# Kernel tuning notes

Hardware: AMD Instinct MI355X
Metric: run time of the kernel (lower is better)

## Reference

```python
import jax, jax.numpy as jnp
import numpy as np

N = 100000
E = 1600000
IN_FEATS = 512
H1, F1 = 8, 8          # layer1: 8 heads x 8 units
H2, F2 = 1, 40         # layer2: 1 head x out_feats
NEG_SLOPE = 0.2


def setup_inputs() -> dict:
    key = jax.random.key(0)
    ks = jax.random.split(key, 12)
    x = jax.random.normal(ks[0], (N, IN_FEATS), dtype=jnp.float32)
    src = jax.random.randint(ks[1], (E,), 0, N, dtype=jnp.int32)
    dst = jax.random.randint(ks[2], (E,), 0, N, dtype=jnp.int32)
    # Xavier-ish init for params
    W1 = jax.random.normal(ks[3], (IN_FEATS, H1 * F1), dtype=jnp.float32) * (1.0 / np.sqrt(IN_FEATS))
    al1 = jax.random.normal(ks[4], (H1, F1), dtype=jnp.float32) * 0.1
    ar1 = jax.random.normal(ks[5], (H1, F1), dtype=jnp.float32) * 0.1
    b1 = jnp.zeros((H1 * F1,), dtype=jnp.float32)
    W2 = jax.random.normal(ks[6], (H1 * F1, H2 * F2), dtype=jnp.float32) * (1.0 / np.sqrt(H1 * F1))
    al2 = jax.random.normal(ks[7], (H2, F2), dtype=jnp.float32) * 0.1
    ar2 = jax.random.normal(ks[8], (H2, F2), dtype=jnp.float32) * 0.1
    b2 = jnp.zeros((H2 * F2,), dtype=jnp.float32)
    return {"x": x, "src": src, "dst": dst,
            "W1": W1, "al1": al1, "ar1": ar1, "b1": b1,
            "W2": W2, "al2": al2, "ar2": ar2, "b2": b2}


def _gat_conv(feat, src, dst, W, al, ar, b, activation):
    """DGL-style GATConv (dropout disabled / eval mode)."""
    n = feat.shape[0]
    heads, fdim = al.shape
    h = (feat @ W).reshape(n, heads, fdim)            # [N, H, F]
    el = jnp.einsum('nhf,hf->nh', h, al)              # [N, H]
    er = jnp.einsum('nhf,hf->nh', h, ar)              # [N, H]
    e = jax.nn.leaky_relu(el[src] + er[dst], NEG_SLOPE)   # [E, H]
    # edge softmax over incoming edges of each dst node (numerically stable)
    m = jax.ops.segment_max(e, dst, num_segments=n)   # [N, H]
    ex = jnp.exp(e - m[dst])
    s = jax.ops.segment_sum(ex, dst, num_segments=n)  # [N, H]
    alpha = ex / s[dst]                               # [E, H]
    msg = h[src] * alpha[:, :, None]                  # [E, H, F]
    rst = jax.ops.segment_sum(msg, dst, num_segments=n)  # [N, H, F]
    rst = rst + b.reshape(1, heads, fdim)
    if activation is not None:
        rst = activation(rst)
    return rst


def reference(x, src, dst, W1, al1, ar1, b1, W2, al2, ar2, b2):
    h1 = _gat_conv(x, src, dst, W1, al1, ar1, b1, jax.nn.elu)   # [N, H1, F1]
    h1 = h1.reshape(x.shape[0], H1 * F1)                        # flatten(1)
    h2 = _gat_conv(h1, src, dst, W2, al2, ar2, b2, None)        # [N, 1, F2]
    logits = h2.mean(axis=1)                                    # [N, F2]
    return jax.nn.log_softmax(logits, axis=1)
```

## Files before the change

### kernel.cpp

```cpp
#include <hip/hip_runtime.h>
#include <cstdint>
#include <cstddef>

#define IN_F 512
#define C1 64
#define NH 8
#define FD 8
#define C2 40
#define NEG 0.2f

typedef __attribute__((ext_vector_type(8))) short bf16x8;
typedef __attribute__((ext_vector_type(4))) float f32x4;

__device__ inline unsigned short f32_to_bf16_rne(float f) {
    unsigned int u = __float_as_uint(f);
    unsigned int r = (u + 0x7FFFu + ((u >> 16) & 1u)) >> 16;
    return (unsigned short)r;
}
__device__ inline float bf16_to_f32(unsigned short s) {
    return __uint_as_float(((unsigned int)s) << 16);
}

__global__ __launch_bounds__(256) void hist_k(const int* __restrict__ dst, int* __restrict__ deg, int E) {
    int e = blockIdx.x * 256 + threadIdx.x;
    if (e < E) atomicAdd(&deg[dst[e]], 1);
}

__global__ __launch_bounds__(1024) void scan_local_k(const int* __restrict__ deg, int* __restrict__ rowp,
                                                     int* __restrict__ bsums, int n) {
    __shared__ int tmp[1024];
    int tx = threadIdx.x;
    int i = blockIdx.x * 1024 + tx;
    int v = (i < n) ? deg[i] : 0;
    tmp[tx] = v;
    __syncthreads();
    for (int d = 1; d < 1024; d <<= 1) {
        int t = (tx >= d) ? tmp[tx - d] : 0;
        __syncthreads();
        tmp[tx] += t;
        __syncthreads();
    }
    if (i < n) rowp[i] = tmp[tx] - v;
    if (tx == 1023) bsums[blockIdx.x] = tmp[tx];
}

__global__ __launch_bounds__(128) void scan_sums_k(int* bsums, int nb) {
    __shared__ int tmp[128];
    int tx = threadIdx.x;
    int v = (tx < nb) ? bsums[tx] : 0;
    tmp[tx] = v;
    __syncthreads();
    for (int d = 1; d < 128; d <<= 1) {
        int t = (tx >= d) ? tmp[tx - d] : 0;
        __syncthreads();
        tmp[tx] += t;
        __syncthreads();
    }
    if (tx < nb) bsums[tx] = tmp[tx] - v;
}

__global__ __launch_bounds__(1024) void scan_add_k(int* rowp, const int* __restrict__ bsums, int n) {
    int i = blockIdx.x * 1024 + threadIdx.x;
    if (i < n) rowp[i] += bsums[blockIdx.x];
}

__global__ __launch_bounds__(256) void scatter_k(const int* __restrict__ src, const int* __restrict__ dst,
                                                 const int* __restrict__ rowp, int* __restrict__ fill,
                                                 int* __restrict__ csr_src, int E) {
    int e = blockIdx.x * 256 + threadIdx.x;
    if (e >= E) return;
    int d = dst[e];
    int p = atomicAdd(&fill[d], 1);
    csr_src[rowp[d] + p] = src[e];
}

__global__ __launch_bounds__(256) void wt_pre_k(const float* __restrict__ W1,
                                                unsigned short* __restrict__ wt_hi,
                                                unsigned short* __restrict__ wt_lo) {
    int id = blockIdx.x * 256 + threadIdx.x;
    if (id >= IN_F * C1) return;
    int col = id & (C1 - 1);
    int k = id >> 6;
    float w = W1[id];
    unsigned short hb = f32_to_bf16_rne(w);
    unsigned short lb = f32_to_bf16_rne(w - bf16_to_f32(hb));
    wt_hi[(size_t)col * IN_F + k] = hb;
    wt_lo[(size_t)col * IN_F + k] = lb;
}

__global__ __launch_bounds__(256) void gemm1_mfma_k(const float* __restrict__ x,
                                                    const unsigned short* __restrict__ wt_hi,
                                                    const unsigned short* __restrict__ wt_lo,
                                                    float* __restrict__ h, int N) {
    __shared__ alignas(16) unsigned short wlds[2][8192];
    const int tid = threadIdx.x;
    const int wave = tid >> 6, lane = tid & 63;
    const int m = lane & 15, q = lane >> 4;
    const int row = blockIdx.x * 64 + wave * 16 + m;
    const int row_c = row < N ? row : N - 1;
    const float* xp = x + (size_t)row_c * IN_F + q * 8;

    f32x4 acc[4];
#pragma unroll
    for (int ct = 0; ct < 4; ct++) acc[ct] = (f32x4){0.f, 0.f, 0.f, 0.f};
    float4 xr[2][4];

#define WLOAD(c, buf)                                                                              \
    {                                                                                              \
        _Pragma("unroll") for (int j_ = 0; j_ < 4; j_++) {                                         \
            int slot_ = j_ * 256 + wave * 64 + lane;                                               \
            const unsigned short* gbase_ = (slot_ < 512) ? wt_hi : wt_lo;                          \
            int s_ = slot_ & 511;                                                                  \
            int col_ = s_ & 63, kq_ = s_ >> 6;                                                     \
            const unsigned short* g_ = gbase_ + (size_t)col_ * IN_F + (c) * 64 + kq_ * 8;          \
            unsigned short* l_ = &wlds[buf][0] + (size_t)(j_ * 256 + wave * 64) * 8;               \
            __builtin_amdgcn_global_load_lds((const __attribute__((address_space(1))) unsigned int*)g_, \
                                             (__attribute__((address_space(3))) unsigned int*)l_,  \
                                             16, 0, 0);                                            \
        }                                                                                          \
    }
#define XLOAD(c, r)                                  \
    {                                                \
        const float* xsrc_ = xp + (c) * 64;          \
        (r)[0] = *(const float4*)(xsrc_);            \
        (r)[1] = *(const float4*)(xsrc_ + 4);        \
        (r)[2] = *(const float4*)(xsrc_ + 32);       \
        (r)[3] = *(const float4*)(xsrc_ + 36);       \
    }

    WLOAD(0, 0);
    XLOAD(0, xr[0]);

    for (int c = 0; c < 8; c++) {
        int p = c & 1;
        __syncthreads();
        if (c < 7) {
            WLOAD(c + 1, p ^ 1);
            XLOAD(c + 1, xr[p ^ 1]);
        }
#pragma unroll
        for (int ki = 0; ki < 2; ki++) {
            float f[8];
            f[0] = xr[p][ki * 2].x; f[1] = xr[p][ki * 2].y; f[2] = xr[p][ki * 2].z; f[3] = xr[p][ki * 2].w;
            f[4] = xr[p][ki * 2 + 1].x; f[5] = xr[p][ki * 2 + 1].y; f[6] = xr[p][ki * 2 + 1].z; f[7] = xr[p][ki * 2 + 1].w;
            unsigned int u[8], lu[8];
#pragma unroll
            for (int j = 0; j < 8; j++) u[j] = __float_as_uint(f[j]);
            union { uint4 u4; bf16x8 v; } H, L;
            H.u4.x = __builtin_amdgcn_perm(u[1], u[0], 0x07060302u);
            H.u4.y = __builtin_amdgcn_perm(u[3], u[2], 0x07060302u);
            H.u4.z = __builtin_amdgcn_perm(u[5], u[4], 0x07060302u);
            H.u4.w = __builtin_amdgcn_perm(u[7], u[6], 0x07060302u);
#pragma unroll
            for (int j = 0; j < 8; j++)
                lu[j] = __float_as_uint(f[j] - __uint_as_float(u[j] & 0xFFFF0000u));
            L.u4.x = __builtin_amdgcn_perm(lu[1], lu[0], 0x07060302u);
            L.u4.y = __builtin_amdgcn_perm(lu[3], lu[2], 0x07060302u);
            L.u4.z = __builtin_amdgcn_perm(lu[5], lu[4], 0x07060302u);
            L.u4.w = __builtin_amdgcn_perm(lu[7], lu[6], 0x07060302u);
            int kq = ki * 4 + q;
#pragma unroll
            for (int ct = 0; ct < 4; ct++) {
                int slot = kq * 64 + ct * 16 + m;
                bf16x8 bh = *(const bf16x8*)&wlds[p][slot * 8];
                bf16x8 bl = *(const bf16x8*)&wlds[p][4096 + slot * 8];
                acc[ct] = __builtin_amdgcn_mfma_f32_16x16x32_bf16(H.v, bh, acc[ct], 0, 0, 0);
                acc[ct] = __builtin_amdgcn_mfma_f32_16x16x32_bf16(L.v, bh, acc[ct], 0, 0, 0);
                acc[ct] = __builtin_amdgcn_mfma_f32_16x16x32_bf16(H.v, bl, acc[ct], 0, 0, 0);
            }
        }
    }
    int rbase = blockIdx.x * 64 + wave * 16 + q * 4;
#pragma unroll
    for (int r = 0; r < 4; r++) {
        int ro = rbase + r;
        if (ro < N) {
#pragma unroll
            for (int ct = 0; ct < 4; ct++)
                h[(size_t)ro * C1 + ct * 16 + m] = acc[ct][r];
        }
    }
#undef WLOAD
#undef XLOAD
}

__global__ __launch_bounds__(256) void attn1_k(const float* __restrict__ h, const float* __restrict__ al,
                                               const float* __restrict__ ar, float* __restrict__ el,
                                               float* __restrict__ er, int N) {
    int idx = blockIdx.x * 256 + threadIdx.x;
    if (idx >= N * NH) return;
    int n = idx >> 3, hd = idx & 7;
    const float4* hp = (const float4*)(h + (size_t)n * C1 + hd * FD);
    const float4* alp = (const float4*)(al + hd * FD);
    const float4* arp = (const float4*)(ar + hd * FD);
    float4 v0 = hp[0], v1 = hp[1];
    float4 a0 = alp[0], a1 = alp[1];
    float4 r0 = arp[0], r1 = arp[1];
    float e_l = v0.x * a0.x + v0.y * a0.y + v0.z * a0.z + v0.w * a0.w +
                v1.x * a1.x + v1.y * a1.y + v1.z * a1.z + v1.w * a1.w;
    float e_r = v0.x * r0.x + v0.y * r0.y + v0.z * r0.z + v0.w * r0.w +
                v1.x * r1.x + v1.y * r1.y + v1.z * r1.z + v1.w * r1.w;
    el[idx] = e_l;
    er[idx] = e_r;
}

__global__ __launch_bounds__(256) void l1_agg_k(const float* __restrict__ h,
                                                const float* __restrict__ el, const float* __restrict__ er,
                                                const int* __restrict__ rowp, const int* __restrict__ deg,
                                                const int* __restrict__ csr_src, const float* __restrict__ b1,
                                                const float* __restrict__ W2, const float* __restrict__ al2,
                                                const float* __restrict__ ar2,
                                                float* __restrict__ h2pre, float* __restrict__ el2o,
                                                float* __restrict__ er2o, int N) {
    __shared__ float ws[C1 * C2];
    __shared__ float hs[32][C1];
    __shared__ float h2s[32][C2];
    __shared__ float a2s[2 * C2];
    int tid = threadIdx.x;
    for (int i = tid; i < C1 * C2; i += 256) ws[i] = W2[i];
    if (tid < C2) a2s[tid] = al2[tid];
    else if (tid < 2 * C2) a2s[tid] = ar2[tid - C2];

    int n0 = blockIdx.x * 32;
    int ln = tid >> 3;
    int hd = tid & 7;
    int n = n0 + ln;
    float4 acc0 = make_float4(0.f, 0.f, 0.f, 0.f);
    float4 acc1 = make_float4(0.f, 0.f, 0.f, 0.f);
    float s = 0.f;
    if (n < N) {
        int start = rowp[n], cnt = deg[n];
        float erd = er[n * NH + hd];
        int i = 0;
        for (; i + 1 < cnt; i += 2) {
            int sn0 = csr_src[start + i];
            int sn1 = csr_src[start + i + 1];
            float e0 = el[sn0 * NH + hd] + erd;
            float e1 = el[sn1 * NH + hd] + erd;
            e0 = e0 > 0.f ? e0 : NEG * e0;
            e1 = e1 > 0.f ? e1 : NEG * e1;
            float w0 = __expf(e0), w1 = __expf(e1);
            s += w0 + w1;
            const float4* hp0 = (const float4*)(h + (size_t)sn0 * C1 + hd * FD);
            const float4* hp1 = (const float4*)(h + (size_t)sn1 * C1 + hd * FD);
            float4 v00 = hp0[0], v01 = hp0[1];
            float4 v10 = hp1[0], v11 = hp1[1];
            acc0.x += w0 * v00.x + w1 * v10.x; acc0.y += w0 * v00.y + w1 * v10.y;
            acc0.z += w0 * v00.z + w1 * v10.z; acc0.w += w0 * v00.w + w1 * v10.w;
            acc1.x += w0 * v01.x + w1 * v11.x; acc1.y += w0 * v01.y + w1 * v11.y;
            acc1.z += w0 * v01.z + w1 * v11.z; acc1.w += w0 * v01.w + w1 * v11.w;
        }
        if (i < cnt) {
            int sn = csr_src[start + i];
            float e = el[sn * NH + hd] + erd;
            e = e > 0.f ? e : NEG * e;
            float w0 = __expf(e);
            s += w0;
            const float4* hp = (const float4*)(h + (size_t)sn * C1 + hd * FD);
            float4 v0 = hp[0], v1 = hp[1];
            acc0.x += w0 * v0.x; acc0.y += w0 * v0.y; acc0.z += w0 * v0.z; acc0.w += w0 * v0.w;
            acc1.x += w0 * v1.x; acc1.y += w0 * v1.y; acc1.z += w0 * v1.z; acc1.w += w0 * v1.w;
        }
    }
    float sinv = (s > 0.f) ? 1.f / s : 0.f;
    const float4* bp = (const float4*)(b1 + hd * FD);
    float4 bb0 = bp[0], bb1 = bp[1];
    float o[8] = {acc0.x * sinv + bb0.x, acc0.y * sinv + bb0.y, acc0.z * sinv + bb0.z, acc0.w * sinv + bb0.w,
                  acc1.x * sinv + bb1.x, acc1.y * sinv + bb1.y, acc1.z * sinv + bb1.z, acc1.w * sinv + bb1.w};
#pragma unroll
    for (int f = 0; f < 8; f++) o[f] = o[f] > 0.f ? o[f] : (__expf(o[f]) - 1.f);
    *(float4*)&hs[ln][hd * FD] = make_float4(o[0], o[1], o[2], o[3]);
    *(float4*)&hs[ln][hd * FD + 4] = make_float4(o[4], o[5], o[6], o[7]);
    __syncthreads();

    for (int oidx = tid; oidx < 32 * C2; oidx += 256) {
        int r = oidx / C2, c = oidx % C2;
        float sum = 0.f;
#pragma unroll
        for (int k = 0; k < C1; k++) sum += hs[r][k] * ws[k * C2 + c];
        h2s[r][c] = sum;
        int nn = n0 + r;
        if (nn < N) h2pre[(size_t)nn * C2 + c] = sum;
    }
    __syncthreads();

    if (tid < 32) {
        int nn = n0 + tid;
        if (nn < N) {
            float e_l = 0.f, e_r = 0.f;
#pragma unroll
            for (int c = 0; c < C2; c++) {
                float v = h2s[tid][c];
                e_l += v * a2s[c];
                e_r += v * a2s[C2 + c];
            }
            el2o[nn] = e_l;
            er2o[nn] = e_r;
        }
    }
}

__global__ __launch_bounds__(256) void l2_fused_k(const float* __restrict__ h2, const float* __restrict__ el,
                                                  const float* __restrict__ er, const int* __restrict__ rowp,
                                                  const int* __restrict__ deg, const int* __restrict__ csr_src,
                                                  const float* __restrict__ b2, float* __restrict__ out, int N) {
    int tid = threadIdx.x;
    int n = blockIdx.x * 32 + (tid >> 3);
    int sub = tid & 7;
    if (n >= N) return;
    int start = rowp[n], cnt = deg[n];
    float erd = er[n];
    float s = 0.f;
    float4 a4 = make_float4(0.f, 0.f, 0.f, 0.f);
    float a1 = 0.f;
    int i = 0;
    for (; i + 1 < cnt; i += 2) {
        int sn0 = csr_src[start + i];
        int sn1 = csr_src[start + i + 1];
        float e0 = el[sn0] + erd, e1 = el[sn1] + erd;
        e0 = e0 > 0.f ? e0 : NEG * e0;
        e1 = e1 > 0.f ? e1 : NEG * e1;
        float w0 = __expf(e0), w1 = __expf(e1);
        s += w0 + w1;
        const float* hp0 = h2 + (size_t)sn0 * C2;
        const float* hp1 = h2 + (size_t)sn1 * C2;
        float4 v0 = *(const float4*)(hp0 + sub * 4);
        float4 v1 = *(const float4*)(hp1 + sub * 4);
        float s0 = hp0[32 + sub], s1 = hp1[32 + sub];
        a4.x += w0 * v0.x + w1 * v1.x; a4.y += w0 * v0.y + w1 * v1.y;
        a4.z += w0 * v0.z + w1 * v1.z; a4.w += w0 * v0.w + w1 * v1.w;
        a1 += w0 * s0 + w1 * s1;
    }
    if (i < cnt) {
        int sn = csr_src[start + i];
        float e = el[sn] + erd;
        e = e > 0.f ? e : NEG * e;
        float w0 = __expf(e);
        s += w0;
        const float* hp = h2 + (size_t)sn * C2;
        float4 v = *(const float4*)(hp + sub * 4);
        a4.x += w0 * v.x; a4.y += w0 * v.y; a4.z += w0 * v.z; a4.w += w0 * v.w;
        a1 += w0 * hp[32 + sub];
    }
    float sinv = (s > 0.f) ? 1.f / s : 0.f;
    float4 bb = *(const float4*)(b2 + sub * 4);
    a4.x = a4.x * sinv + bb.x; a4.y = a4.y * sinv + bb.y;
    a4.z = a4.z * sinv + bb.z; a4.w = a4.w * sinv + bb.w;
    a1 = a1 * sinv + b2[32 + sub];
    float mx = fmaxf(fmaxf(fmaxf(a4.x, a4.y), fmaxf(a4.z, a4.w)), a1);
#pragma unroll
    for (int off = 1; off < 8; off <<= 1) mx = fmaxf(mx, __shfl_xor(mx, off, 8));
    float se = __expf(a4.x - mx) + __expf(a4.y - mx) + __expf(a4.z - mx) + __expf(a4.w - mx) + __expf(a1 - mx);
#pragma unroll
    for (int off = 1; off < 8; off <<= 1) se += __shfl_xor(se, off, 8);
    float ls = __logf(se) + mx;
    float* op = out + (size_t)n * C2;
    *(float4*)(op + sub * 4) = make_float4(a4.x - ls, a4.y - ls, a4.z - ls, a4.w - ls);
    op[32 + sub] = a1 - ls;
}

extern "C" void kernel_launch(void* const* d_in, const int* in_sizes, int n_in,
                              void* d_out, int out_size, void* d_ws, size_t ws_size,
                              hipStream_t stream) {
    (void)n_in; (void)out_size; (void)ws_size;
    const float* x   = (const float*)d_in[0];
    const int*   src = (const int*)d_in[1];
    const int*   dst = (const int*)d_in[2];
    const float* W1  = (const float*)d_in[3];
    const float* al1 = (const float*)d_in[4];
    const float* ar1 = (const float*)d_in[5];
    const float* b1  = (const float*)d_in[6];
    const float* W2  = (const float*)d_in[7];
    const float* al2 = (const float*)d_in[8];
    const float* ar2 = (const float*)d_in[9];
    const float* b2  = (const float*)d_in[10];
    float* out = (float*)d_out;
    const int N = in_sizes[0] / IN_F;
    const int E = in_sizes[1];

    char* w = (char*)d_ws;
    auto alloc = [&](size_t bytes) -> char* {
        char* p = w;
        w += (bytes + 255) & ~(size_t)255;
        return p;
    };
    int* deg     = (int*)alloc((size_t)N * 4);
    int* fill    = (int*)alloc((size_t)N * 4);
    int* rowp    = (int*)alloc((size_t)N * 4);
    int* bsums   = (int*)alloc(512);
    int* csr_src = (int*)alloc((size_t)E * 4);
    unsigned short* wt_hi = (unsigned short*)alloc((size_t)IN_F * C1 * 2);
    unsigned short* wt_lo = (unsigned short*)alloc((size_t)IN_F * C1 * 2);
    float* h1pre = (float*)alloc((size_t)N * C1 * 4);
    float* el1   = (float*)alloc((size_t)N * NH * 4);
    float* er1   = (float*)alloc((size_t)N * NH * 4);
    float* h2pre = (float*)alloc((size_t)N * C2 * 4);
    float* el2   = (float*)alloc((size_t)N * 4);
    float* er2   = (float*)alloc((size_t)N * 4);

    hipMemsetAsync(deg, 0, (size_t)N * 4, stream);
    hipMemsetAsync(fill, 0, (size_t)N * 4, stream);

    int ebl = (E + 255) / 256;
    int nb = (N + 1023) / 1024;
    hist_k<<<ebl, 256, 0, stream>>>(dst, deg, E);
    scan_local_k<<<nb, 1024, 0, stream>>>(deg, rowp, bsums, N);
    scan_sums_k<<<1, 128, 0, stream>>>(bsums, nb);
    scan_add_k<<<nb, 1024, 0, stream>>>(rowp, bsums, N);
    scatter_k<<<ebl, 256, 0, stream>>>(src, dst, rowp, fill, csr_src, E);

    wt_pre_k<<<(IN_F * C1 + 255) / 256, 256, 0, stream>>>(W1, wt_hi, wt_lo);
    gemm1_mfma_k<<<(N + 63) / 64, 256, 0, stream>>>(x, wt_hi, wt_lo, h1pre, N);
    attn1_k<<<(N * NH + 255) / 256, 256, 0, stream>>>(h1pre, al1, ar1, el1, er1, N);
    l1_agg_k<<<(N + 31) / 32, 256, 0, stream>>>(h1pre, el1, er1, rowp, deg, csr_src, b1,
                                                W2, al2, ar2, h2pre, el2, er2, N);
    l2_fused_k<<<(N + 31) / 32, 256, 0, stream>>>(h2pre, el2, er2, rowp, deg, csr_src, b2, out, N);
}
```

Measured before the change: 648.9 us.

## Split layer-1 aggregation into wave-per-node gather and separate GEMM2 kernel

Layer-1 aggregation now runs one 64-lane wave per destination node, with each lane owning one output channel, so each neighbour row is read as one coalesced 256-byte line. The W2 projection and layer-2 attention logits move into a separate kernel that tiles 64 nodes per block. CSR construction records the atomic slot in the histogram pass, which removes the second atomic pass and the fill buffer. The layer-2 gather loop is unrolled by four to keep more loads in flight. In exchange it adds an N×64 intermediate write and read, an extra kernel launch, an E-sized pos buffer, and redundant el/exp work across the 8 lanes of each head.

```diff
diff --git a/kernel.cpp b/kernel.cpp
--- a/kernel.cpp
+++ b/kernel.cpp
@@ -21,9 +21,10 @@
     return __uint_as_float(((unsigned int)s) << 16);
 }
 
-__global__ __launch_bounds__(256) void hist_k(const int* __restrict__ dst, int* __restrict__ deg, int E) {
+__global__ __launch_bounds__(256) void hist_k(const int* __restrict__ dst, int* __restrict__ deg,
+                                              int* __restrict__ pos, int E) {
     int e = blockIdx.x * 256 + threadIdx.x;
-    if (e < E) atomicAdd(&deg[dst[e]], 1);
+    if (e < E) pos[e] = atomicAdd(&deg[dst[e]], 1);
 }
 
 __global__ __launch_bounds__(1024) void scan_local_k(const int* __restrict__ deg, int* __restrict__ rowp,
@@ -65,13 +66,11 @@
 }
 
 __global__ __launch_bounds__(256) void scatter_k(const int* __restrict__ src, const int* __restrict__ dst,
-                                                 const int* __restrict__ rowp, int* __restrict__ fill,
+                                                 const int* __restrict__ rowp, const int* __restrict__ pos,
                                                  int* __restrict__ csr_src, int E) {
     int e = blockIdx.x * 256 + threadIdx.x;
     if (e >= E) return;
-    int d = dst[e];
-    int p = atomicAdd(&fill[d], 1);
-    csr_src[rowp[d] + p] = src[e];
+    csr_src[rowp[dst[e]] + pos[e]] = src[e];
 }
 
 __global__ __launch_bounds__(256) void wt_pre_k(const float* __restrict__ W1,
@@ -204,77 +203,75 @@
     er[idx] = e_r;
 }
 
-__global__ __launch_bounds__(256) void l1_agg_k(const float* __restrict__ h,
-                                                const float* __restrict__ el, const float* __restrict__ er,
-                                                const int* __restrict__ rowp, const int* __restrict__ deg,
-                                                const int* __restrict__ csr_src, const float* __restrict__ b1,
-                                                const float* __restrict__ W2, const float* __restrict__ al2,
-                                                const float* __restrict__ ar2,
-                                                float* __restrict__ h2pre, float* __restrict__ el2o,
-                                                float* __restrict__ er2o, int N) {
+__global__ __launch_bounds__(256) void l1_wave_k(const float* __restrict__ h,
+                                                 const float* __restrict__ el, const float* __restrict__ er,
+                                                 const int* __restrict__ rowp, const int* __restrict__ deg,
+                                                 const int* __restrict__ csr_src, const float* __restrict__ b1,
+                                                 float* __restrict__ h1out, int N) {
+    int n = (blockIdx.x * 256 + threadIdx.x) >> 6;
+    if (n >= N) return;
+    int lane = threadIdx.x & 63;
+    int hg = lane >> 3;
+    int start = rowp[n], cnt = deg[n];
+    float erd = er[n * NH + hg];
+    float acc = 0.f, s = 0.f;
+    int i = 0;
+    for (; i + 4 <= cnt; i += 4) {
+        const int* cp = csr_src + start + i;
+        int sn0 = cp[0], sn1 = cp[1], sn2 = cp[2], sn3 = cp[3];
+        float e0 = el[sn0 * NH + hg];
+        float e1 = el[sn1 * NH + hg];
+        float e2 = el[sn2 * NH + hg];
+        float e3 = el[sn3 * NH + hg];
+        float v0 = h[(size_t)sn0 * C1 + lane];
+        float v1 = h[(size_t)sn1 * C1 + lane];
+        float v2 = h[(size_t)sn2 * C1 + lane];
+        float v3 = h[(size_t)sn3 * C1 + lane];
+        e0 += erd; e1 += erd; e2 += erd; e3 += erd;
+        e0 = e0 > 0.f ? e0 : NEG * e0;
+        e1 = e1 > 0.f ? e1 : NEG * e1;
+        e2 = e2 > 0.f ? e2 : NEG * e2;
+        e3 = e3 > 0.f ? e3 : NEG * e3;
+        float w0 = __expf(e0), w1 = __expf(e1), w2 = __expf(e2), w3 = __expf(e3);
+        s += (w0 + w1) + (w2 + w3);
+        acc += w0 * v0 + w1 * v1 + w2 * v2 + w3 * v3;
+    }
+    for (; i < cnt; i++) {
+        int sn = csr_src[start + i];
+        float e = el[sn * NH + hg] + erd;
+        e = e > 0.f ? e : NEG * e;
+        float w0 = __expf(e);
+        s += w0;
+        acc += w0 * h[(size_t)sn * C1 + lane];
+    }
+    float sinv = (s > 0.f) ? 1.f / s : 0.f;
+    float o = acc * sinv + b1[lane];
+    o = o > 0.f ? o : (__expf(o) - 1.f);
+    h1out[(size_t)n * C1 + lane] = o;
+}
+
+__global__ __launch_bounds__(256) void gemm2_attn2_k(const float* __restrict__ h1, const float* __restrict__ W2,
+                                                     const float* __restrict__ al2, const float* __restrict__ ar2,
+                                                     float* __restrict__ h2pre, float* __restrict__ el2,
+                                                     float* __restrict__ er2, int N) {
     __shared__ float ws[C1 * C2];
-    __shared__ float hs[32][C1];
-    __shared__ float h2s[32][C2];
+    __shared__ float hs[64][C1];
+    __shared__ float h2s[64][C2];
     __shared__ float a2s[2 * C2];
-    int tid = threadIdx.x;
-    for (int i = tid; i < C1 * C2; i += 256) ws[i] = W2[i];
-    if (tid < C2) a2s[tid] = al2[tid];
-    else if (tid < 2 * C2) a2s[tid] = ar2[tid - C2];
-
-    int n0 = blockIdx.x * 32;
-    int ln = tid >> 3;
-    int hd = tid & 7;
-    int n = n0 + ln;
-    float4 acc0 = make_float4(0.f, 0.f, 0.f, 0.f);
-    float4 acc1 = make_float4(0.f, 0.f, 0.f, 0.f);
-    float s = 0.f;
-    if (n < N) {
-        int start = rowp[n], cnt = deg[n];
-        float erd = er[n * NH + hd];
-        int i = 0;
-        for (; i + 1 < cnt; i += 2) {
-            int sn0 = csr_src[start + i];
-            int sn1 = csr_src[start + i + 1];
-            float e0 = el[sn0 * NH + hd] + erd;
-            float e1 = el[sn1 * NH + hd] + erd;
-            e0 = e0 > 0.f ? e0 : NEG * e0;
-            e1 = e1 > 0.f ? e1 : NEG * e1;
-            float w0 = __expf(e0), w1 = __expf(e1);
-            s += w0 + w1;
-            const float4* hp0 = (const float4*)(h + (size_t)sn0 * C1 + hd * FD);
-            const float4* hp1 = (const float4*)(h + (size_t)sn1 * C1 + hd * FD);
-            float4 v00 = hp0[0], v01 = hp0[1];
-            float4 v10 = hp1[0], v11 = hp1[1];
-            acc0.x += w0 * v00.x + w1 * v10.x; acc0.y += w0 * v00.y + w1 * v10.y;
-            acc0.z += w0 * v00.z + w1 * v10.z; acc0.w += w0 * v00.w + w1 * v10.w;
-            acc1.x += w0 * v01.x + w1 * v11.x; acc1.y += w0 * v01.y + w1 * v11.y;
-            acc1.z += w0 * v01.z + w1 * v11.z; acc1.w += w0 * v01.w + w1 * v11.w;
-        }
-        if (i < cnt) {
-            int sn = csr_src[start + i];
-            float e = el[sn * NH + hd] + erd;
-            e = e > 0.f ? e : NEG * e;
-            float w0 = __expf(e);
-            s += w0;
-            const float4* hp = (const float4*)(h + (size_t)sn * C1 + hd * FD);
-            float4 v0 = hp[0], v1 = hp[1];
-            acc0.x += w0 * v0.x; acc0.y += w0 * v0.y; acc0.z += w0 * v0.z; acc0.w += w0 * v0.w;
-            acc1.x += w0 * v1.x; acc1.y += w0 * v1.y; acc1.z += w0 * v1.z; acc1.w += w0 * v1.w;
-        }
-    }
-    float sinv = (s > 0.f) ? 1.f / s : 0.f;
-    const float4* bp = (const float4*)(b1 + hd * FD);
-    float4 bb0 = bp[0], bb1 = bp[1];
-    float o[8] = {acc0.x * sinv + bb0.x, acc0.y * sinv + bb0.y, acc0.z * sinv + bb0.z, acc0.w * sinv + bb0.w,
-                  acc1.x * sinv + bb1.x, acc1.y * sinv + bb1.y, acc1.z * sinv + bb1.z, acc1.w * sinv + bb1.w};
-#pragma unroll
-    for (int f = 0; f < 8; f++) o[f] = o[f] > 0.f ? o[f] : (__expf(o[f]) - 1.f);
-    *(float4*)&hs[ln][hd * FD] = make_float4(o[0], o[1], o[2], o[3]);
-    *(float4*)&hs[ln][hd * FD + 4] = make_float4(o[4], o[5], o[6], o[7]);
+    int t = threadIdx.x;
+    int n0 = blockIdx.x * 64;
+    for (int i = t; i < C1 * C2; i += 256) ws[i] = W2[i];
+    if (t < C2) a2s[t] = al2[t];
+    else if (t < 2 * C2) a2s[t] = ar2[t - C2];
+    for (int i = t; i < 64 * 16; i += 256) {
+        int r = i >> 4, c4 = i & 15;
+        int n = n0 + r;
+        float4 v = (n < N) ? *(const float4*)(h1 + (size_t)n * C1 + c4 * 4) : make_float4(0.f, 0.f, 0.f, 0.f);
+        *(float4*)&hs[r][c4 * 4] = v;
+    }
     __syncthreads();
-
-    for (int oidx = tid; oidx < 32 * C2; oidx += 256) {
-        int r = oidx / C2, c = oidx % C2;
+    for (int o = t; o < 64 * C2; o += 256) {
+        int r = o / C2, c = o % C2;
         float sum = 0.f;
 #pragma unroll
         for (int k = 0; k < C1; k++) sum += hs[r][k] * ws[k * C2 + c];
@@ -283,19 +280,18 @@
         if (nn < N) h2pre[(size_t)nn * C2 + c] = sum;
     }
     __syncthreads();
-
-    if (tid < 32) {
-        int nn = n0 + tid;
+    if (t < 64) {
+        int nn = n0 + t;
         if (nn < N) {
             float e_l = 0.f, e_r = 0.f;
 #pragma unroll
             for (int c = 0; c < C2; c++) {
-                float v = h2s[tid][c];
+                float v = h2s[t][c];
                 e_l += v * a2s[c];
                 e_r += v * a2s[C2 + c];
             }
-            el2o[nn] = e_l;
-            er2o[nn] = e_r;
+            el2[nn] = e_l;
+            er2[nn] = e_r;
         }
     }
 }
@@ -314,24 +310,33 @@
     float4 a4 = make_float4(0.f, 0.f, 0.f, 0.f);
     float a1 = 0.f;
     int i = 0;
-    for (; i + 1 < cnt; i += 2) {
-        int sn0 = csr_src[start + i];
-        int sn1 = csr_src[start + i + 1];
-        float e0 = el[sn0] + erd, e1 = el[sn1] + erd;
+    for (; i + 4 <= cnt; i += 4) {
+        const int* cp = csr_src + start + i;
+        int sn0 = cp[0], sn1 = cp[1], sn2 = cp[2], sn3 = cp[3];
+        float e0 = el[sn0], e1 = el[sn1], e2 = el[sn2], e3 = el[sn3];
+        const float* hp0 = h2 + (size_t)sn0 * C2;
+        const float* hp1 = h2 + (size_t)sn1 * C2;
+        const float* hp2 = h2 + (size_t)sn2 * C2;
+        const float* hp3 = h2 + (size_t)sn3 * C2;
+        float4 v0 = *(const float4*)(hp0 + sub * 4);
+        float4 v1 = *(const float4*)(hp1 + sub * 4);
+        float4 v2 = *(const float4*)(hp2 + sub * 4);
+        float4 v3 = *(const float4*)(hp3 + sub * 4);
+        float s0 = hp0[32 + sub], s1 = hp1[32 + sub], s2 = hp2[32 + sub], s3 = hp3[32 + sub];
+        e0 += erd; e1 += erd; e2 += erd; e3 += erd;
         e0 = e0 > 0.f ? e0 : NEG * e0;
         e1 = e1 > 0.f ? e1 : NEG * e1;
-        float w0 = __expf(e0), w1 = __expf(e1);
-        s += w0 + w1;
-        const float* hp0 = h2 + (size_t)sn0 * C2;
-        const float* hp1 = h2 + (size_t)sn1 * C2;
-        float4 v0 = *(const float4*)(hp0 + sub * 4);
-        float4 v1 = *(const float4*)(hp1 + sub * 4);
-        float s0 = hp0[32 + sub], s1 = hp1[32 + sub];
-        a4.x += w0 * v0.x + w1 * v1.x; a4.y += w0 * v0.y + w1 * v1.y;
-        a4.z += w0 * v0.z + w1 * v1.z; a4.w += w0 * v0.w + w1 * v1.w;
-        a1 += w0 * s0 + w1 * s1;
-    }
-    if (i < cnt) {
+        e2 = e2 > 0.f ? e2 : NEG * e2;
+        e3 = e3 > 0.f ? e3 : NEG * e3;
+        float w0 = __expf(e0), w1 = __expf(e1), w2 = __expf(e2), w3 = __expf(e3);
+        s += (w0 + w1) + (w2 + w3);
+        a4.x += w0 * v0.x + w1 * v1.x + w2 * v2.x + w3 * v3.x;
+        a4.y += w0 * v0.y + w1 * v1.y + w2 * v2.y + w3 * v3.y;
+        a4.z += w0 * v0.z + w1 * v1.z + w2 * v2.z + w3 * v3.z;
+        a4.w += w0 * v0.w + w1 * v1.w + w2 * v2.w + w3 * v3.w;
+        a1 += w0 * s0 + w1 * s1 + w2 * s2 + w3 * s3;
+    }
+    for (; i < cnt; i++) {
         int sn = csr_src[start + i];
         float e = el[sn] + erd;
         e = e > 0.f ? e : NEG * e;
@@ -385,34 +390,34 @@
         return p;
     };
     int* deg     = (int*)alloc((size_t)N * 4);
-    int* fill    = (int*)alloc((size_t)N * 4);
     int* rowp    = (int*)alloc((size_t)N * 4);
     int* bsums   = (int*)alloc(512);
+    int* pos     = (int*)alloc((size_t)E * 4);
     int* csr_src = (int*)alloc((size_t)E * 4);
     unsigned short* wt_hi = (unsigned short*)alloc((size_t)IN_F * C1 * 2);
     unsigned short* wt_lo = (unsigned short*)alloc((size_t)IN_F * C1 * 2);
     float* h1pre = (float*)alloc((size_t)N * C1 * 4);
     float* el1   = (float*)alloc((size_t)N * NH * 4);
     float* er1   = (float*)alloc((size_t)N * NH * 4);
+    float* h1    = (float*)alloc((size_t)N * C1 * 4);
     float* h2pre = (float*)alloc((size_t)N * C2 * 4);
     float* el2   = (float*)alloc((size_t)N * 4);
     float* er2   = (float*)alloc((size_t)N * 4);
 
     hipMemsetAsync(deg, 0, (size_t)N * 4, stream);
-    hipMemsetAsync(fill, 0, (size_t)N * 4, stream);
 
     int ebl = (E + 255) / 256;
     int nb = (N + 1023) / 1024;
-    hist_k<<<ebl, 256, 0, stream>>>(dst, deg, E);
+    hist_k<<<ebl, 256, 0, stream>>>(dst, deg, pos, E);
     scan_local_k<<<nb, 1024, 0, stream>>>(deg, rowp, bsums, N);
     scan_sums_k<<<1, 128, 0, stream>>>(bsums, nb);
     scan_add_k<<<nb, 1024, 0, stream>>>(rowp, bsums, N);
-    scatter_k<<<ebl, 256, 0, stream>>>(src, dst, rowp, fill, csr_src, E);
+    scatter_k<<<ebl, 256, 0, stream>>>(src, dst, rowp, pos, csr_src, E);
 
     wt_pre_k<<<(IN_F * C1 + 255) / 256, 256, 0, stream>>>(W1, wt_hi, wt_lo);
     gemm1_mfma_k<<<(N + 63) / 64, 256, 0, stream>>>(x, wt_hi, wt_lo, h1pre, N);
     attn1_k<<<(N * NH + 255) / 256, 256, 0, stream>>>(h1pre, al1, ar1, el1, er1, N);
-    l1_agg_k<<<(N + 31) / 32, 256, 0, stream>>>(h1pre, el1, er1, rowp, deg, csr_src, b1,
-                                                W2, al2, ar2, h2pre, el2, er2, N);
+    l1_wave_k<<<(N * 64 + 255) / 256, 256, 0, stream>>>(h1pre, el1, er1, rowp, deg, csr_src, b1, h1, N);
+    gemm2_attn2_k<<<(N + 63) / 64, 256, 0, stream>>>(h1, W2, al2, ar2, h2pre, el2, er2, N);
     l2_fused_k<<<(N + 31) / 32, 256, 0, stream>>>(h2pre, el2, er2, rowp, deg, csr_src, b2, out, N);
 }
```

Result: faster. 635.6 us (-2.0%).
